# Kernel tuning notes

Measured on AMD Instinct MI355X. Metric: run time of the kernel, lower is better.

## Reference

```python
import jax, jax.numpy as jnp
import numpy as np

H = 8
NUM_GRAPHS = 128
EDGE_DIM = 147

def _glorot(k, shape, fan_in):
    return jax.random.normal(k, shape, jnp.float32) * (1.0 / np.sqrt(fan_in))

def setup_inputs():
    ks = jax.random.split(jax.random.key(0), 28)
    N, E = 50000, 200000
    inp = {}
    inp['x'] = jax.random.normal(ks[0], (N, 64), jnp.float32)
    inp['edge_attr'] = jax.random.uniform(ks[1], (E, EDGE_DIM), dtype=jnp.float32)
    dims = [(64, 64), (512, 64), (512, 32)]  # (in_channels, per-head out) per GATConv layer
    ki = 2
    for i in range(3):
        cin, c = dims[i]
        hc = H * c
        inp['W%d' % i] = _glorot(ks[ki], (hc, cin), cin); ki += 1
        inp['We%d' % i] = _glorot(ks[ki], (hc, EDGE_DIM), EDGE_DIM); ki += 1
        inp['as%d' % i] = _glorot(ks[ki], (1, H, c), c); ki += 1
        inp['ad%d' % i] = _glorot(ks[ki], (1, H, c), c); ki += 1
        inp['ae%d' % i] = _glorot(ks[ki], (1, H, c), c); ki += 1
        inp['b%d' % i] = jnp.zeros((hc,), jnp.float32); ki += 1
    inp['Wc'] = _glorot(ks[ki], (32, 256), 256)
    inp['bc'] = jnp.zeros((32,), jnp.float32)
    inp['edge_index'] = jax.random.randint(ks[ki + 1], (2, E), 0, N)
    inp['batch'] = jnp.sort(jax.random.randint(ks[ki + 2], (N,), 0, NUM_GRAPHS))
    return inp

def _gat_layer(x, src, dst, ea, W, We, a_s, a_d, a_e, b):
    # PyG GATConv (concat=True, eval mode): project, per-edge attention logits,
    # softmax over incoming edges of each destination node, weighted scatter-sum, bias.
    N = x.shape[0]
    HC = W.shape[0]
    C = HC // H
    xp = (x @ W.T).reshape(N, H, C)              # [N,H,C]
    ep = (ea @ We.T).reshape(-1, H, C)           # [E,H,C]
    logits = (xp * a_s).sum(-1)[src] + (xp * a_d).sum(-1)[dst] + (ep * a_e).sum(-1)
    logits = jax.nn.leaky_relu(logits, 0.2)      # [E,H]
    mx = jax.ops.segment_max(logits, dst, num_segments=N)
    mx = jnp.where(jnp.isfinite(mx), mx, 0.0)
    ex = jnp.exp(logits - mx[dst])
    denom = jax.ops.segment_sum(ex, dst, num_segments=N)
    attn = ex / (denom[dst] + 1e-16)             # [E,H]
    out = jax.ops.segment_sum(xp[src] * attn[:, :, None], dst, num_segments=N)
    return out.reshape(N, HC) + b

def _forward(x, edge_attr, params, Wc, bc, edge_index, batch):
    N = x.shape[0]
    src, dst = edge_index[0], edge_index[1]
    # GATConv add_self_loops=True, fill_value='mean': self-loop edge attr is
    # the per-node mean of incoming edge attrs (0 for isolated nodes).
    ones_e = jnp.ones((src.shape[0],), x.dtype)
    deg = jax.ops.segment_sum(ones_e, dst, num_segments=N)
    loop_attr = jax.ops.segment_sum(edge_attr, dst, num_segments=N) / jnp.clip(deg, 1.0)[:, None]
    ar = jnp.arange(N)
    src_f = jnp.concatenate([src, ar])
    dst_f = jnp.concatenate([dst, ar])
    ea_f = jnp.concatenate([edge_attr, loop_attr], axis=0)
    h = x
    for i, p in enumerate(params):
        h = _gat_layer(h, src_f, dst_f, ea_f, *p)
        if i < len(params) - 1:
            h = jax.nn.elu(h)  # dropout is identity in eval
    # batch indices are sorted and contiguous, so the unique->contiguous remap
    # in the original forward is the identity; global mean pool:
    cnt = jax.ops.segment_sum(jnp.ones((N,), h.dtype), batch, num_segments=NUM_GRAPHS)
    pooled = jax.ops.segment_sum(h, batch, num_segments=NUM_GRAPHS) / jnp.clip(cnt, 1.0)[:, None]
    return pooled @ Wc.T + bc

def reference(x, edge_attr, W0, We0, as0, ad0, ae0, b0, W1, We1, as1, ad1, ae1, b1, W2, We2, as2, ad2, ae2, b2, Wc, bc, edge_index, batch):
    params = [(W0, We0, as0, ad0, ae0, b0), (W1, We1, as1, ad1, ae1, b1), (W2, We2, as2, ad2, ae2, b2)]
    return _forward(x, edge_attr, params, Wc, bc, edge_index, batch)
```

## Files before the change

### kernel.cpp

```cpp
#include <hip/hip_runtime.h>
#include <hip/hip_bf16.h>
#include <math.h>

typedef __attribute__((ext_vector_type(8))) _Float16 f16x8;
typedef __attribute__((ext_vector_type(4))) _Float16 f16x4;
typedef __attribute__((ext_vector_type(4))) float f32x4;

#define AS1(p) ((const __attribute__((address_space(1))) void*)(p))
#define AS3(p) ((__attribute__((address_space(3))) void*)(p))

__device__ __forceinline__ float leaky02(float x){ return x > 0.f ? x : 0.2f*x; }
__device__ __forceinline__ ushort f2h(float f){ _Float16 h = (_Float16)f; return *(ushort*)&h; }
__device__ __forceinline__ float h2f(ushort u){ _Float16 h = *(_Float16*)&u; return (float)h; }

__global__ void count_kernel(const int* __restrict__ dst, int* __restrict__ cnt, int E){
  int e = blockIdx.x*blockDim.x + threadIdx.x;
  if (e < E) atomicAdd(&cnt[dst[e]], 1);
}

__global__ void scanA_kernel(const int* __restrict__ cnt, int* __restrict__ bsum, int N){
  __shared__ int sd[256];
  int i = blockIdx.x*256 + threadIdx.x;
  sd[threadIdx.x] = (i<N) ? cnt[i] : 0;
  __syncthreads();
  for (int off=128; off>0; off>>=1){
    if (threadIdx.x < off) sd[threadIdx.x] += sd[threadIdx.x+off];
    __syncthreads();
  }
  if (threadIdx.x==0) bsum[blockIdx.x] = sd[0];
}
__global__ void scanB_kernel(int* __restrict__ bsum, int B){
  __shared__ int sd[256];
  int t = threadIdx.x;
  int v = (t<B) ? bsum[t] : 0;
  sd[t] = v;
  __syncthreads();
  for (int off=1; off<256; off<<=1){
    int u = (t>=off) ? sd[t-off] : 0;
    __syncthreads();
    sd[t] += u;
    __syncthreads();
  }
  if (t<B) bsum[t] = sd[t] - v;
}
__global__ void scanC_kernel(const int* __restrict__ cnt, const int* __restrict__ bsum,
                             int* __restrict__ row_ptr, int N){
  __shared__ int sd[256];
  int i = blockIdx.x*256 + threadIdx.x;
  int v = (i<N) ? cnt[i] : 0;
  sd[threadIdx.x] = v;
  __syncthreads();
  for (int off=1; off<256; off<<=1){
    int u = (threadIdx.x>=off) ? sd[threadIdx.x-off] : 0;
    __syncthreads();
    sd[threadIdx.x] += u;
    __syncthreads();
  }
  if (i < N) row_ptr[i+1] = sd[threadIdx.x] + bsum[blockIdx.x];
  if (i == 0) row_ptr[0] = 0;
}

__global__ void scatter_kernel(const int* __restrict__ src, const int* __restrict__ dst,
                               const int* __restrict__ row_ptr, int* __restrict__ cursor,
                               int* __restrict__ epos, int* __restrict__ csr_src, int E){
  int e = blockIdx.x*blockDim.x + threadIdx.x;
  if (e < E){
    int d = dst[e];
    int pos = row_ptr[d] + atomicAdd(&cursor[d], 1);
    epos[e] = pos;
    csr_src[pos] = src[e];
  }
}

__global__ void conv4_kernel(const float* __restrict__ p0, const float* __restrict__ p1,
                             const float* __restrict__ p2, const float* __restrict__ p3,
                             ushort* __restrict__ q0, ushort* __restrict__ q1,
                             ushort* __restrict__ q2, ushort* __restrict__ q3,
                             int n0, int n1, int n2, int n3){
  int i = blockIdx.x*256 + threadIdx.x;
  const float* src; ushort* dst; int loc;
  if (i < n0){ src=p0; dst=q0; loc=i; }
  else if (i < n0+n1){ src=p1; dst=q1; loc=i-n0; }
  else if (i < n0+n1+n2){ src=p2; dst=q2; loc=i-n0-n1; }
  else if (i < n0+n1+n2+n3){ src=p3; dst=q3; loc=i-n0-n1-n2; }
  else return;
  float4 v = reinterpret_cast<const float4*>(src)[loc];
  ushort4 o; o.x=f2h(v.x); o.y=f2h(v.y); o.z=f2h(v.z); o.w=f2h(v.w);
  reinterpret_cast<ushort4*>(dst)[loc] = o;
}

__global__ void wfold_direct_kernel(const float* __restrict__ We0, const float* __restrict__ ae0,
                                    const float* __restrict__ We1, const float* __restrict__ ae1,
                                    const float* __restrict__ We2, const float* __restrict__ ae2,
                                    ushort* __restrict__ Bh){
  int t = blockIdx.x*256 + threadIdx.x;
  if (t >= 32*160) return;
  int j = t/160, d = t%160;
  float s = 0.f;
  if (j < 24 && d < 147){
    int l = j >> 3, h = j & 7;
    const float* We = (l==0) ? We0 : (l==1) ? We1 : We2;
    const float* ae = (l==0) ? ae0 : (l==1) ? ae1 : ae2;
    int C = (l==2) ? 32 : 64;
    for (int c=0;c<C;c++) s = fmaf(We[(size_t)(h*C+c)*147 + d], ae[h*C+c], s);
  }
  Bh[t] = f2h(s);
}

__global__ __launch_bounds__(256) void edge_alpha_mfma_kernel(const float* __restrict__ ea, const ushort* __restrict__ Bh,
                                                              const int* __restrict__ epos,
                                                              float* __restrict__ aEc, int E){
  int wave = threadIdx.x>>6, lane = threadIdx.x&63;
  int fr = lane&15, fq = lane>>4;
  int m0 = blockIdx.x*64 + wave*16;
  f32x4 acc0 = {0.f,0.f,0.f,0.f}, acc1 = {0.f,0.f,0.f,0.f};
  int row = m0 + fr; if (row > E-1) row = E-1;
  const float*  ar = ea + (size_t)row*147;
  const ushort* b0 = Bh + (size_t)fr*160      + fq*8;
  const ushort* b1 = Bh + (size_t)(16+fr)*160 + fq*8;
  #pragma unroll
  for (int k=0;k<160;k+=32){
    int c0 = k + fq*8;
    f16x8 a;
    #pragma unroll
    for (int u=0;u<8;u++){
      float v = (c0+u < 147) ? ar[c0+u] : 0.f;
      a[u] = (_Float16)v;
    }
    f16x8 p = *(const f16x8*)(b0 + k);
    f16x8 q = *(const f16x8*)(b1 + k);
    acc0 = __builtin_amdgcn_mfma_f32_16x16x32_f16(a, p, acc0, 0, 0, 0);
    acc1 = __builtin_amdgcn_mfma_f32_16x16x32_f16(a, q, acc1, 0, 0, 0);
  }
  #pragma unroll
  for (int j=0;j<4;j++){
    int r = m0 + fq*4 + j;
    if (r < E){
      int p = epos[r];
      aEc[(size_t)p*24 + fr] = acc0[j];
      if (fr < 8) aEc[(size_t)p*24 + 16 + fr] = acc1[j];
    }
  }
}

__global__ __launch_bounds__(192) void loop_alpha_all_kernel(const float* __restrict__ aEc, const int* __restrict__ row_ptr,
                                                             float* __restrict__ loopAE, int N){
  int n = blockIdx.x*8 + threadIdx.x/24;
  int j = threadIdx.x%24;
  if (n >= N) return;
  int row = row_ptr[n], end = row_ptr[n+1];
  float s = 0.f;
  for (int i=row;i<end;i++) s += aEc[(size_t)i*24 + j];
  loopAE[(size_t)n*24 + j] = s / fmaxf((float)(end-row), 1.0f);
}

template<int CPH>
__global__ __launch_bounds__(256) void gemm_mfma_kernel(const ushort* __restrict__ A, const ushort* __restrict__ B,
                                                        ushort* __restrict__ C,
                                                        const float* __restrict__ a_s, const float* __restrict__ a_d,
                                                        float* __restrict__ alphaS, float* __restrict__ alphaD,
                                                        int M, int Nn, int K, int NY){
  __shared__ ushort lds[128*64*4];
  int nwg = gridDim.x;
  int bid = blockIdx.x;
  int q8 = nwg >> 3, r8 = nwg & 7;
  int xcd = bid & 7, loc = bid >> 3;
  int swz = (xcd < r8 ? xcd*(q8+1) : r8*(q8+1) + (xcd-r8)*q8) + loc;
  int m0 = (swz / NY) * 128, n0 = (swz % NY) * 128;

  int wave = threadIdx.x >> 6, lane = threadIdx.x & 63;
  int wr = wave >> 1, wc = wave & 1;
  f32x4 acc[4][4];
  #pragma unroll
  for (int m=0;m<4;m++)
    #pragma unroll
    for (int n=0;n<4;n++) acc[m][n] = (f32x4){0.f,0.f,0.f,0.f};

  int lrow = lane >> 3;
  int lcol = lane & 7;
  int srcChunk = lcol ^ lrow;
  int fr = lane & 15;
  int fq = lane >> 4;

  auto stage = [&](int buf, int k0){
    ushort* As = lds + buf*(128*64*2);
    ushort* Bs = As + 128*64;
    #pragma unroll
    for (int qq=0;qq<4;qq++){
      int r = qq*32 + wave*8 + lrow;
      int gr = m0 + r; if (gr > M-1) gr = M-1;
      __builtin_amdgcn_global_load_lds(AS1(A + (size_t)gr*K + k0 + srcChunk*8), AS3(&As[(qq*32 + wave*8)*64]), 16, 0, 0);
      __builtin_amdgcn_global_load_lds(AS1(B + (size_t)(n0 + r)*K + k0 + srcChunk*8), AS3(&Bs[(qq*32 + wave*8)*64]), 16, 0, 0);
    }
  };

  int nt = K >> 6;
  stage(0, 0);
  int buf = 0;
  for (int t=0; t<nt; ++t){
    if (t+1 < nt){
      stage(buf^1, (t+1)<<6);
      asm volatile("s_waitcnt vmcnt(8)" ::: "memory");
    } else {
      asm volatile("s_waitcnt vmcnt(0)" ::: "memory");
    }
    __builtin_amdgcn_s_barrier();
    __builtin_amdgcn_sched_barrier(0);
    const ushort* As = lds + buf*(128*64*2);
    const ushort* Bs = As + 128*64;
    #pragma unroll
    for (int kk=0; kk<64; kk+=32){
      f16x8 a[4], b[4];
      #pragma unroll
      for (int m=0;m<4;m++){
        int Ra = wr*64 + m*16 + fr;
        int ch = ((kk>>3) + fq) ^ (Ra & 7);
        a[m] = *(const f16x8*)&As[Ra*64 + ch*8];
      }
      #pragma unroll
      for (int n=0;n<4;n++){
        int Rb = wc*64 + n*16 + fr;
        int ch = ((kk>>3) + fq) ^ (Rb & 7);
        b[n] = *(const f16x8*)&Bs[Rb*64 + ch*8];
      }
      #pragma unroll
      for (int m=0;m<4;m++)
        #pragma unroll
        for (int n=0;n<4;n++)
          acc[m][n] = __builtin_amdgcn_mfma_f32_16x16x32_f16(a[m], b[n], acc[m][n], 0, 0, 0);
    }
    __builtin_amdgcn_s_barrier();
    buf ^= 1;
  }

  {
    ushort* Cs = lds;
    #pragma unroll
    for (int m=0;m<4;m++)
      #pragma unroll
      for (int j=0;j<4;j++){
        int rr = wr*64 + m*16 + fq*4 + j;
        #pragma unroll
        for (int n=0;n<4;n++)
          Cs[rr*128 + wc*64 + n*16 + fr] = f2h(acc[m][n][j]);
      }
    __builtin_amdgcn_s_barrier();
    int rbase = threadIdx.x >> 4;
    int cc = (threadIdx.x & 15)*8;
    #pragma unroll
    for (int p=0;p<8;p++){
      int rr = p*16 + rbase;
      int grow = m0 + rr;
      if (grow < M)
        *(f16x8*)(C + (size_t)grow*Nn + n0 + cc) = *(const f16x8*)&Cs[rr*128 + cc];
    }
  }

  int colbase = n0 + wc*64;
  if (CPH == 64){
    int head = colbase >> 6;
    float asv[4], adv[4];
    #pragma unroll
    for (int n=0;n<4;n++){ int cih = n*16 + fr; asv[n] = a_s[head*64 + cih]; adv[n] = a_d[head*64 + cih]; }
    #pragma unroll
    for (int m=0;m<4;m++){
      float ps[4] = {0,0,0,0}, pd[4] = {0,0,0,0};
      #pragma unroll
      for (int n=0;n<4;n++)
        #pragma unroll
        for (int j=0;j<4;j++){ ps[j] = fmaf(acc[m][n][j], asv[n], ps[j]); pd[j] = fmaf(acc[m][n][j], adv[n], pd[j]); }
      #pragma unroll
      for (int off=1; off<16; off<<=1)
        #pragma unroll
        for (int j=0;j<4;j++){ ps[j] += __shfl_xor(ps[j], off); pd[j] += __shfl_xor(pd[j], off); }
      if (fr == 0){
        #pragma unroll
        for (int j=0;j<4;j++){
          int row = m0 + wr*64 + m*16 + fq*4 + j;
          if (row < M){ alphaS[(size_t)row*8 + head] = ps[j]; alphaD[(size_t)row*8 + head] = pd[j]; }
        }
      }
    }
  } else {
    int head0 = colbase >> 5;
    float asv[4], adv[4];
    #pragma unroll
    for (int n=0;n<4;n++){
      int h = head0 + (n>>1);
      int cih = (n&1)*16 + fr;
      asv[n] = a_s[h*32 + cih]; adv[n] = a_d[h*32 + cih];
    }
    #pragma unroll
    for (int m=0;m<4;m++){
      float psA[4]={0,0,0,0}, pdA[4]={0,0,0,0}, psB[4]={0,0,0,0}, pdB[4]={0,0,0,0};
      #pragma unroll
      for (int j=0;j<4;j++){
        #pragma unroll
        for (int n=0;n<2;n++){ psA[j] = fmaf(acc[m][n][j], asv[n], psA[j]); pdA[j] = fmaf(acc[m][n][j], adv[n], pdA[j]); }
        #pragma unroll
        for (int n=2;n<4;n++){ psB[j] = fmaf(acc[m][n][j], asv[n], psB[j]); pdB[j] = fmaf(acc[m][n][j], adv[n], pdB[j]); }
      }
      #pragma unroll
      for (int off=1; off<16; off<<=1)
        #pragma unroll
        for (int j=0;j<4;j++){
          psA[j] += __shfl_xor(psA[j], off); pdA[j] += __shfl_xor(pdA[j], off);
          psB[j] += __shfl_xor(psB[j], off); pdB[j] += __shfl_xor(pdB[j], off);
        }
      if (fr == 0){
        #pragma unroll
        for (int j=0;j<4;j++){
          int row = m0 + wr*64 + m*16 + fq*4 + j;
          if (row < M){
            alphaS[(size_t)row*8 + head0]     = psA[j]; alphaD[(size_t)row*8 + head0]     = pdA[j];
            alphaS[(size_t)row*8 + head0 + 1] = psB[j]; alphaD[(size_t)row*8 + head0 + 1] = pdB[j];
          }
        }
      }
    }
  }
}

template<int V> struct vecT;
template<> struct vecT<8>{ typedef f16x8 T; };
template<> struct vecT<4>{ typedef f16x4 T; };

template<int V>
__device__ __forceinline__ void rowfma(typename vecT<V>::T v, float ex, float* acc){
  #pragma unroll
  for (int j=0;j<V;j++) acc[j] = fmaf(ex, (float)v[j], acc[j]);
}

template<int HC, int ELU>
__global__ __launch_bounds__(256) void aggregate_kernel(
    const ushort* __restrict__ xh, const float* __restrict__ alphaS, const float* __restrict__ alphaD,
    const float* __restrict__ aEc, const float* __restrict__ loopAE,
    const int* __restrict__ row_ptr, const int* __restrict__ csr_src,
    const float* __restrict__ bias, ushort* __restrict__ out, int N, int off){
  constexpr int V = HC/64;
  typedef typename vecT<V>::T vec;
  int w = blockIdx.x*4 + (threadIdx.x>>6);
  int nA = w*2, nB = w*2+1;
  if (nA >= N) return;
  bool hasB = (nB < N);
  int lane = threadIdx.x & 63;
  int h = lane >> 3;
  int cofs = V*lane;

  float adnA = alphaD[(size_t)nA*8 + h];
  float accA[V], accB[V];
  float denA, denB = 0.f;
  {
    float exs = __expf(leaky02(alphaS[(size_t)nA*8 + h] + adnA + loopAE[(size_t)nA*24 + off + h]));
    denA = exs;
    #pragma unroll
    for (int j=0;j<V;j++) accA[j] = 0.f;
    rowfma<V>(*(const vec*)(xh + (size_t)nA*HC + cofs), exs, accA);
  }
  #pragma unroll
  for (int j=0;j<V;j++) accB[j] = 0.f;
  float adnB = 0.f;
  int iA = row_ptr[nA], eAe = row_ptr[nA+1];
  int iB = eAe, eBe = eAe;
  if (hasB){
    adnB = alphaD[(size_t)nB*8 + h];
    float exs = __expf(leaky02(alphaS[(size_t)nB*8 + h] + adnB + loopAE[(size_t)nB*24 + off + h]));
    denB = exs;
    rowfma<V>(*(const vec*)(xh + (size_t)nB*HC + cofs), exs, accB);
    eBe = row_ptr[nB+1];
  }

  bool run = (iA+1 < eAe) && (iB+1 < eBe);
  int sA0=0,sA1=0,sB0=0,sB1=0;
  float gA0=0,gA1=0,gB0=0,gB1=0, tA0=0,tA1=0,tB0=0,tB1=0;
  vec vA0{}, vA1{}, vB0{}, vB1{};
  if (run){
    sA0=csr_src[iA]; sA1=csr_src[iA+1]; sB0=csr_src[iB]; sB1=csr_src[iB+1];
    gA0=alphaS[(size_t)sA0*8+h]; gA1=alphaS[(size_t)sA1*8+h];
    gB0=alphaS[(size_t)sB0*8+h]; gB1=alphaS[(size_t)sB1*8+h];
    tA0=aEc[(size_t)iA*24+off+h]; tA1=aEc[(size_t)(iA+1)*24+off+h];
    tB0=aEc[(size_t)iB*24+off+h]; tB1=aEc[(size_t)(iB+1)*24+off+h];
    vA0=*(const vec*)(xh+(size_t)sA0*HC+cofs); vA1=*(const vec*)(xh+(size_t)sA1*HC+cofs);
    vB0=*(const vec*)(xh+(size_t)sB0*HC+cofs); vB1=*(const vec*)(xh+(size_t)sB1*HC+cofs);
  }
  while (run){
    int jA = iA+2, jB = iB+2;
    bool nrun = (jA+1 < eAe) && (jB+1 < eBe);
    vec cA0=vA0, cA1=vA1, cB0=vB0, cB1=vB1;
    float eA0=__expf(leaky02(gA0+adnA+tA0));
    float eA1=__expf(leaky02(gA1+adnA+tA1));
    float eB0=__expf(leaky02(gB0+adnB+tB0));
    float eB1=__expf(leaky02(gB1+adnB+tB1));
    if (nrun){
      sA0=csr_src[jA]; sA1=csr_src[jA+1]; sB0=csr_src[jB]; sB1=csr_src[jB+1];
      gA0=alphaS[(size_t)sA0*8+h]; gA1=alphaS[(size_t)sA1*8+h];
      gB0=alphaS[(size_t)sB0*8+h]; gB1=alphaS[(size_t)sB1*8+h];
      tA0=aEc[(size_t)jA*24+off+h]; tA1=aEc[(size_t)(jA+1)*24+off+h];
      tB0=aEc[(size_t)jB*24+off+h]; tB1=aEc[(size_t)(jB+1)*24+off+h];
      vA0=*(const vec*)(xh+(size_t)sA0*HC+cofs); vA1=*(const vec*)(xh+(size_t)sA1*HC+cofs);
      vB0=*(const vec*)(xh+(size_t)sB0*HC+cofs); vB1=*(const vec*)(xh+(size_t)sB1*HC+cofs);
    }
    denA += eA0 + eA1; denB += eB0 + eB1;
    rowfma<V>(cA0, eA0, accA); rowfma<V>(cA1, eA1, accA);
    rowfma<V>(cB0, eB0, accB); rowfma<V>(cB1, eB1, accB);
    iA = jA; iB = jB;
    run = nrun;
  }
  for (; iA+1 < eAe; iA += 2){
    int s0 = csr_src[iA], s1 = csr_src[iA+1];
    float g0 = alphaS[(size_t)s0*8+h], g1 = alphaS[(size_t)s1*8+h];
    float t0 = aEc[(size_t)iA*24+off+h], t1 = aEc[(size_t)(iA+1)*24+off+h];
    vec v0 = *(const vec*)(xh+(size_t)s0*HC+cofs);
    vec v1 = *(const vec*)(xh+(size_t)s1*HC+cofs);
    float e0 = __expf(leaky02(g0+adnA+t0));
    float e1 = __expf(leaky02(g1+adnA+t1));
    denA += e0 + e1;
    rowfma<V>(v0, e0, accA); rowfma<V>(v1, e1, accA);
  }
  if (iA < eAe){
    int s = csr_src[iA];
    float g = alphaS[(size_t)s*8+h];
    float t = aEc[(size_t)iA*24+off+h];
    vec v = *(const vec*)(xh+(size_t)s*HC+cofs);
    float e = __expf(leaky02(g+adnA+t));
    denA += e;
    rowfma<V>(v, e, accA);
  }
  for (; iB+1 < eBe; iB += 2){
    int s0 = csr_src[iB], s1 = csr_src[iB+1];
    float g0 = alphaS[(size_t)s0*8+h], g1 = alphaS[(size_t)s1*8+h];
    float t0 = aEc[(size_t)iB*24+off+h], t1 = aEc[(size_t)(iB+1)*24+off+h];
    vec v0 = *(const vec*)(xh+(size_t)s0*HC+cofs);
    vec v1 = *(const vec*)(xh+(size_t)s1*HC+cofs);
    float e0 = __expf(leaky02(g0+adnB+t0));
    float e1 = __expf(leaky02(g1+adnB+t1));
    denB += e0 + e1;
    rowfma<V>(v0, e0, accB); rowfma<V>(v1, e1, accB);
  }
  if (iB < eBe){
    int s = csr_src[iB];
    float g = alphaS[(size_t)s*8+h];
    float t = aEc[(size_t)iB*24+off+h];
    vec v = *(const vec*)(xh+(size_t)s*HC+cofs);
    float e = __expf(leaky02(g+adnB+t));
    denB += e;
    rowfma<V>(v, e, accB);
  }

  float invA = 1.f/(denA + 1e-16f);
  {
    vec ov;
    #pragma unroll
    for (int j=0;j<V;j++){
      float o = accA[j]*invA + bias[cofs + j];
      if (ELU) o = (o > 0.f) ? o : (__expf(o) - 1.f);
      ov[j] = (_Float16)o;
    }
    *(vec*)(out + (size_t)nA*HC + cofs) = ov;
  }
  if (hasB){
    float invB = 1.f/(denB + 1e-16f);
    vec ov;
    #pragma unroll
    for (int j=0;j<V;j++){
      float o = accB[j]*invB + bias[cofs + j];
      if (ELU) o = (o > 0.f) ? o : (__expf(o) - 1.f);
      ov[j] = (_Float16)o;
    }
    *(vec*)(out + (size_t)nB*HC + cofs) = ov;
  }
}

__global__ __launch_bounds__(256) void pool_sum_kernel(const ushort* __restrict__ h, const int* __restrict__ batch,
                                                       float* __restrict__ pooled, int N){
  __shared__ int bsh[128];
  int i0 = blockIdx.x*128;
  int i1 = min(i0+128, N);
  if (threadIdx.x < i1-i0) bsh[threadIdx.x] = batch[i0+threadIdx.x];
  __syncthreads();
  int c = threadIdx.x;
  int gprev = bsh[0];
  float s = 0.f;
  for (int i=i0;i<i1;i++){
    int g = bsh[i-i0];
    if (g != gprev){ atomicAdd(&pooled[gprev*256 + c], s); s = 0.f; gprev = g; }
    s += h2f(h[(size_t)i*256 + c]);
  }
  atomicAdd(&pooled[gprev*256 + c], s);
}

__device__ __forceinline__ int lower_bound_i(const int* a, int n, int key){
  int lo=0, hi=n;
  while (lo<hi){ int mid=(lo+hi)>>1; if (a[mid]<key) lo=mid+1; else hi=mid; }
  return lo;
}

__global__ void final_kernel(const float* __restrict__ pooled, const int* __restrict__ batch,
                             const float* __restrict__ Wc, const float* __restrict__ bc,
                             float* __restrict__ out, int N){
  int g = blockIdx.x; int j = threadIdx.x;
  if (j >= 32) return;
  int start = lower_bound_i(batch, N, g);
  int end   = lower_bound_i(batch, N, g+1);
  float invc = 1.f / fmaxf((float)(end-start), 1.f);
  const float* p = pooled + g*256;
  const float* w = Wc + (size_t)j*256;
  float s = 0.f;
  for (int c=0;c<256;c++) s = fmaf(p[c], w[c], s);
  out[g*32 + j] = s*invc + bc[j];
}

extern "C" void kernel_launch(void* const* d_in, const int* in_sizes, int n_in,
                              void* d_out, int out_size, void* d_ws, size_t ws_size,
                              hipStream_t stream){
  (void)n_in; (void)out_size; (void)ws_size;
  const float* x   = (const float*)d_in[0];
  const float* ea  = (const float*)d_in[1];
  const float* Wt[3]  = {(const float*)d_in[2],  (const float*)d_in[8],  (const float*)d_in[14]};
  const float* Wet[3] = {(const float*)d_in[3],  (const float*)d_in[9],  (const float*)d_in[15]};
  const float* ast[3] = {(const float*)d_in[4],  (const float*)d_in[10], (const float*)d_in[16]};
  const float* adt[3] = {(const float*)d_in[5],  (const float*)d_in[11], (const float*)d_in[17]};
  const float* aet[3] = {(const float*)d_in[6],  (const float*)d_in[12], (const float*)d_in[18]};
  const float* bt[3]  = {(const float*)d_in[7],  (const float*)d_in[13], (const float*)d_in[19]};
  const float* Wc  = (const float*)d_in[20];
  const float* bc  = (const float*)d_in[21];
  const int* ei    = (const int*)d_in[22];
  const int* batch = (const int*)d_in[23];
  int N = in_sizes[0] / 64;
  int E = in_sizes[1] / 147;
  const int* srcp = ei;
  const int* dstp = ei + E;

  char* w = (char*)d_ws;
  size_t off = 0;
  auto carve = [&](size_t bytes)->char*{ char* p = w + off; off += (bytes + 255) & ~(size_t)255; return p; };
  ushort* xh     = (ushort*)carve((size_t)N*512*2);
  ushort* hb     = (ushort*)carve((size_t)N*512*2);
  ushort* xb     = (ushort*)carve((size_t)N*64*2);
  ushort* Wb[3];
  Wb[0] = (ushort*)carve((size_t)512*64*2);
  Wb[1] = (ushort*)carve((size_t)512*512*2);
  Wb[2] = (ushort*)carve((size_t)256*512*2);
  ushort* wfBh   = (ushort*)carve((size_t)32*160*2);
  float*  aEc    = (float*) carve((size_t)E*24*4);
  float*  loopAE = (float*) carve((size_t)N*24*4);
  float*  alphaS = (float*) carve((size_t)N*8*4);
  float*  alphaD = (float*) carve((size_t)N*8*4);
  int*    row_ptr= (int*)   carve((size_t)(N+1)*4);
  int*    epos   = (int*)   carve((size_t)E*4);
  int*    csr_src= (int*)   carve((size_t)E*4);
  int*    bsum   = (int*)   carve((size_t)256*4);
  char*   zbase  = carve(0);
  float*  pooled = (float*) carve((size_t)128*256*4);
  int*    cnt    = (int*)   carve((size_t)N*4);
  int*    cursor = (int*)   carve((size_t)N*4);
  char*   zend   = carve(0);

  hipMemsetAsync(zbase, 0, (size_t)(zend - zbase), stream);

  int nscan = (N+255)/256;
  count_kernel  <<<(E+255)/256, 256, 0, stream>>>(dstp, cnt, E);
  scanA_kernel  <<<nscan, 256, 0, stream>>>(cnt, bsum, N);
  scanB_kernel  <<<1, 256, 0, stream>>>(bsum, nscan);
  scanC_kernel  <<<nscan, 256, 0, stream>>>(cnt, bsum, row_ptr, N);
  scatter_kernel<<<(E+255)/256, 256, 0, stream>>>(srcp, dstp, row_ptr, cursor, epos, csr_src, E);

  wfold_direct_kernel<<<(32*160+255)/256, 256, 0, stream>>>(Wet[0], aet[0], Wet[1], aet[1], Wet[2], aet[2], wfBh);

  conv4_kernel<<<(N*16 + 8192 + 65536 + 32768 + 255)/256, 256, 0, stream>>>(
      x, Wt[0], Wt[1], Wt[2], xb, Wb[0], Wb[1], Wb[2], N*16, 8192, 65536, 32768);

  edge_alpha_mfma_kernel<<<(E+63)/64, 256, 0, stream>>>(ea, wfBh, epos, aEc, E);
  loop_alpha_all_kernel <<<(N+7)/8, 192, 0, stream>>>(aEc, row_ptr, loopAE, N);

  const int HCs[3]  = {512, 512, 256};
  const int CINs[3] = {64, 512, 512};
  int nrow = (N+127)/128;
  for (int l=0; l<3; l++){
    int HC = HCs[l], CIN = CINs[l];
    const ushort* Ain = (l==0) ? xb : hb;
    int NY = HC/128;
    int nwg = nrow * NY;
    if (HC==512) gemm_mfma_kernel<64><<<nwg, 256, 0, stream>>>(Ain, Wb[l], xh, ast[l], adt[l], alphaS, alphaD, N, HC, CIN, NY);
    else         gemm_mfma_kernel<32><<<nwg, 256, 0, stream>>>(Ain, Wb[l], xh, ast[l], adt[l], alphaS, alphaD, N, HC, CIN, NY);
    int ablocks = (N + 7) / 8;
    if (l==0)
      aggregate_kernel<512,1><<<ablocks, 256, 0, stream>>>(xh, alphaS, alphaD, aEc, loopAE, row_ptr, csr_src, bt[l], hb, N, 0);
    else if (l==1)
      aggregate_kernel<512,1><<<ablocks, 256, 0, stream>>>(xh, alphaS, alphaD, aEc, loopAE, row_ptr, csr_src, bt[l], hb, N, 8);
    else
      aggregate_kernel<256,0><<<ablocks, 256, 0, stream>>>(xh, alphaS, alphaD, aEc, loopAE, row_ptr, csr_src, bt[l], hb, N, 16);
  }
  pool_sum_kernel<<<(N+127)/128, 256, 0, stream>>>(hb, batch, pooled, N);
  final_kernel<<<128, 64, 0, stream>>>(pooled, batch, Wc, bc, (float*)d_out, N);
}
```

Baseline: 423.7 us.

## Aggregate layer-0 in 64-dim input space before projecting with per-head GEMM

For the first GAT layer, the attention source/destination logits are computed from folded vectors (W0^T a_s, W0^T a_d) applied to the 64-dim input. Per-edge exponentials are precomputed, and messages are aggregated over the raw 64-dim features per head instead of the 512-dim projected features. A block-diagonal MFMA GEMM then applies each head's projection with bias and ELU. This cuts gather traffic in layer 0 by reading 64-wide rows instead of 512-wide ones. The cost is extra kernels, a csr_dst array, and the skipped max subtraction in the softmax, which risks overflow for large logits.

```diff
diff --git a/kernel.cpp b/kernel.cpp
--- a/kernel.cpp
+++ b/kernel.cpp
@@ -62,13 +62,15 @@
 
 __global__ void scatter_kernel(const int* __restrict__ src, const int* __restrict__ dst,
                                const int* __restrict__ row_ptr, int* __restrict__ cursor,
-                               int* __restrict__ epos, int* __restrict__ csr_src, int E){
+                               int* __restrict__ epos, int* __restrict__ csr_src,
+                               int* __restrict__ csr_dst, int E){
   int e = blockIdx.x*blockDim.x + threadIdx.x;
   if (e < E){
     int d = dst[e];
     int pos = row_ptr[d] + atomicAdd(&cursor[d], 1);
     epos[e] = pos;
     csr_src[pos] = src[e];
+    csr_dst[pos] = d;
   }
 }
 
@@ -107,6 +109,37 @@
   Bh[t] = f2h(s);
 }
 
+__global__ void fold_vsd_kernel(const float* __restrict__ W0, const float* __restrict__ a_s,
+                                const float* __restrict__ a_d, float* __restrict__ vs, float* __restrict__ vd){
+  int t = blockIdx.x*256 + threadIdx.x;
+  if (t >= 512) return;
+  int h = t>>6, d = t&63;
+  float ss=0.f, sd=0.f;
+  for (int c=0;c<64;c++){
+    float w = W0[(size_t)(h*64+c)*64 + d];
+    ss = fmaf(w, a_s[h*64+c], ss);
+    sd = fmaf(w, a_d[h*64+c], sd);
+  }
+  vs[t]=ss; vd[t]=sd;
+}
+
+__global__ void alpha_sd_x_kernel(const ushort* __restrict__ xb, const float* __restrict__ vs, const float* __restrict__ vd,
+                                  float* __restrict__ alphaS, float* __restrict__ alphaD, int N){
+  int t = blockIdx.x*256 + threadIdx.x;
+  if (t >= N*8) return;
+  int n = t>>3, h = t&7;
+  const ushort* xr = xb + (size_t)n*64;
+  const float* vsr = vs + h*64;
+  const float* vdr = vd + h*64;
+  float ss=0.f, sd=0.f;
+  for (int d0=0; d0<64; d0+=8){
+    f16x8 v = *(const f16x8*)(xr + d0);
+    #pragma unroll
+    for (int u=0;u<8;u++){ float f = (float)v[u]; ss = fmaf(f, vsr[d0+u], ss); sd = fmaf(f, vdr[d0+u], sd); }
+  }
+  alphaS[t]=ss; alphaD[t]=sd;
+}
+
 __global__ __launch_bounds__(256) void edge_alpha_mfma_kernel(const float* __restrict__ ea, const ushort* __restrict__ Bh,
                                                               const int* __restrict__ epos,
                                                               float* __restrict__ aEc, int E){
@@ -152,6 +185,147 @@
   float s = 0.f;
   for (int i=row;i<end;i++) s += aEc[(size_t)i*24 + j];
   loopAE[(size_t)n*24 + j] = s / fmaxf((float)(end-row), 1.0f);
+}
+
+__global__ __launch_bounds__(256) void edge_exp_kernel(
+    const float* __restrict__ alphaS, const float* __restrict__ alphaD,
+    const float* __restrict__ aEc, const float* __restrict__ loopAE,
+    const int* __restrict__ csr_src, const int* __restrict__ csr_dst,
+    float* __restrict__ exv_csr, float* __restrict__ selfEx,
+    int E, int N, int off){
+  int t = blockIdx.x*256 + threadIdx.x;
+  if (t < E*8){
+    int i = t >> 3, h = t & 7;
+    int s = csr_src[i], n = csr_dst[i];
+    float v = leaky02(alphaS[(size_t)s*8+h] + alphaD[(size_t)n*8+h] + aEc[(size_t)i*24 + off + h]);
+    exv_csr[t] = __expf(v);
+  } else if (t < (E+N)*8){
+    int u = t - E*8;
+    int n = u >> 3, h = u & 7;
+    float v = leaky02(alphaS[(size_t)n*8+h] + alphaD[(size_t)n*8+h] + loopAE[(size_t)n*24 + off + h]);
+    selfEx[u] = __expf(v);
+  }
+}
+
+__device__ __forceinline__ void acc8(const float4& lo, const float4& hi, float xv, float* acc, float* den){
+  acc[0]=fmaf(lo.x,xv,acc[0]); acc[1]=fmaf(lo.y,xv,acc[1]); acc[2]=fmaf(lo.z,xv,acc[2]); acc[3]=fmaf(lo.w,xv,acc[3]);
+  acc[4]=fmaf(hi.x,xv,acc[4]); acc[5]=fmaf(hi.y,xv,acc[5]); acc[6]=fmaf(hi.z,xv,acc[6]); acc[7]=fmaf(hi.w,xv,acc[7]);
+  den[0]+=lo.x; den[1]+=lo.y; den[2]+=lo.z; den[3]+=lo.w;
+  den[4]+=hi.x; den[5]+=hi.y; den[6]+=hi.z; den[7]+=hi.w;
+}
+
+__global__ __launch_bounds__(256) void aggregate_in_kernel(
+    const ushort* __restrict__ xb, const float* __restrict__ exv, const float* __restrict__ selfEx,
+    const int* __restrict__ row_ptr, const int* __restrict__ csr_src,
+    ushort* __restrict__ agg, int N){
+  int w = blockIdx.x*4 + (threadIdx.x>>6);
+  int nA = w*2, nB = w*2+1;
+  if (nA >= N) return;
+  bool hasB = (nB < N);
+  int d = threadIdx.x & 63;
+  float accA[8], accB[8], denA[8], denB[8];
+  {
+    float4 e0 = *(const float4*)&selfEx[(size_t)nA*8];
+    float4 e1 = *(const float4*)&selfEx[(size_t)nA*8+4];
+    float xs = h2f(xb[(size_t)nA*64 + d]);
+    #pragma unroll
+    for (int h=0;h<8;h++){ accA[h]=0.f; denA[h]=0.f; }
+    acc8(e0, e1, xs, accA, denA);
+  }
+  #pragma unroll
+  for (int h=0;h<8;h++){ accB[h]=0.f; denB[h]=0.f; }
+  if (hasB){
+    float4 e0 = *(const float4*)&selfEx[(size_t)nB*8];
+    float4 e1 = *(const float4*)&selfEx[(size_t)nB*8+4];
+    float xs = h2f(xb[(size_t)nB*64 + d]);
+    acc8(e0, e1, xs, accB, denB);
+  }
+  int iA = row_ptr[nA], eA = row_ptr[nA+1];
+  int iB = eA, eB = eA;
+  if (hasB) eB = row_ptr[nB+1];
+  while (iA+1 < eA && iB+1 < eB){
+    int sA0=csr_src[iA], sA1=csr_src[iA+1], sB0=csr_src[iB], sB1=csr_src[iB+1];
+    float xA0=h2f(xb[(size_t)sA0*64+d]), xA1=h2f(xb[(size_t)sA1*64+d]);
+    float xB0=h2f(xb[(size_t)sB0*64+d]), xB1=h2f(xb[(size_t)sB1*64+d]);
+    float4 a00=*(const float4*)&exv[(size_t)iA*8],     a01=*(const float4*)&exv[(size_t)iA*8+4];
+    float4 a10=*(const float4*)&exv[(size_t)(iA+1)*8], a11=*(const float4*)&exv[(size_t)(iA+1)*8+4];
+    float4 b00=*(const float4*)&exv[(size_t)iB*8],     b01=*(const float4*)&exv[(size_t)iB*8+4];
+    float4 b10=*(const float4*)&exv[(size_t)(iB+1)*8], b11=*(const float4*)&exv[(size_t)(iB+1)*8+4];
+    acc8(a00, a01, xA0, accA, denA); acc8(a10, a11, xA1, accA, denA);
+    acc8(b00, b01, xB0, accB, denB); acc8(b10, b11, xB1, accB, denB);
+    iA += 2; iB += 2;
+  }
+  for (; iA+1 < eA; iA += 2){
+    int s0=csr_src[iA], s1=csr_src[iA+1];
+    float x0=h2f(xb[(size_t)s0*64+d]), x1=h2f(xb[(size_t)s1*64+d]);
+    float4 a0=*(const float4*)&exv[(size_t)iA*8],     a1=*(const float4*)&exv[(size_t)iA*8+4];
+    float4 c0=*(const float4*)&exv[(size_t)(iA+1)*8], c1=*(const float4*)&exv[(size_t)(iA+1)*8+4];
+    acc8(a0, a1, x0, accA, denA); acc8(c0, c1, x1, accA, denA);
+  }
+  if (iA < eA){
+    int s=csr_src[iA];
+    float x0=h2f(xb[(size_t)s*64+d]);
+    float4 a0=*(const float4*)&exv[(size_t)iA*8], a1=*(const float4*)&exv[(size_t)iA*8+4];
+    acc8(a0, a1, x0, accA, denA);
+  }
+  for (; iB+1 < eB; iB += 2){
+    int s0=csr_src[iB], s1=csr_src[iB+1];
+    float x0=h2f(xb[(size_t)s0*64+d]), x1=h2f(xb[(size_t)s1*64+d]);
+    float4 a0=*(const float4*)&exv[(size_t)iB*8],     a1=*(const float4*)&exv[(size_t)iB*8+4];
+    float4 c0=*(const float4*)&exv[(size_t)(iB+1)*8], c1=*(const float4*)&exv[(size_t)(iB+1)*8+4];
+    acc8(a0, a1, x0, accB, denB); acc8(c0, c1, x1, accB, denB);
+  }
+  if (iB < eB){
+    int s=csr_src[iB];
+    float x0=h2f(xb[(size_t)s*64+d]);
+    float4 a0=*(const float4*)&exv[(size_t)iB*8], a1=*(const float4*)&exv[(size_t)iB*8+4];
+    acc8(a0, a1, x0, accB, denB);
+  }
+  #pragma unroll
+  for (int h=0;h<8;h++)
+    agg[(size_t)nA*512 + h*64 + d] = f2h(accA[h] / (denA[h] + 1e-16f));
+  if (hasB){
+    #pragma unroll
+    for (int h=0;h<8;h++)
+      agg[(size_t)nB*512 + h*64 + d] = f2h(accB[h] / (denB[h] + 1e-16f));
+  }
+}
+
+__global__ __launch_bounds__(256) void bd_gemm_kernel(const ushort* __restrict__ agg, const ushort* __restrict__ W0,
+                                                      const float* __restrict__ b0, ushort* __restrict__ out, int N){
+  int head = blockIdx.y;
+  int wave = threadIdx.x>>6, lane = threadIdx.x&63;
+  int fr = lane&15, fq = lane>>4;
+  int r0 = blockIdx.x*64 + wave*16;
+  f32x4 acc[4];
+  #pragma unroll
+  for (int ct=0;ct<4;ct++) acc[ct] = (f32x4){0.f,0.f,0.f,0.f};
+  int arow = r0 + fr; if (arow > N-1) arow = N-1;
+  const ushort* abase = agg + (size_t)arow*512 + head*64 + fq*8;
+  const ushort* bbase = W0 + (size_t)(head*64)*64 + fq*8;
+  #pragma unroll
+  for (int kk=0; kk<64; kk+=32){
+    f16x8 a = *(const f16x8*)(abase + kk);
+    #pragma unroll
+    for (int ct=0; ct<4; ct++){
+      f16x8 b = *(const f16x8*)(bbase + (size_t)(ct*16+fr)*64 + kk);
+      acc[ct] = __builtin_amdgcn_mfma_f32_16x16x32_f16(a, b, acc[ct], 0, 0, 0);
+    }
+  }
+  #pragma unroll
+  for (int ct=0;ct<4;ct++){
+    int col = head*64 + ct*16 + fr;
+    float bb = b0[col];
+    #pragma unroll
+    for (int j=0;j<4;j++){
+      int row = r0 + fq*4 + j;
+      if (row < N){
+        float o = acc[ct][j] + bb;
+        o = (o > 0.f) ? o : (__expf(o) - 1.f);
+        out[(size_t)row*512 + col] = f2h(o);
+      }
+    }
+  }
 }
 
 template<int CPH>
@@ -546,9 +720,14 @@
   float*  loopAE = (float*) carve((size_t)N*24*4);
   float*  alphaS = (float*) carve((size_t)N*8*4);
   float*  alphaD = (float*) carve((size_t)N*8*4);
+  float*  exv    = (float*) carve((size_t)E*8*4);
+  float*  selfEx = (float*) carve((size_t)N*8*4);
+  float*  vs     = (float*) carve((size_t)8*64*4);
+  float*  vd     = (float*) carve((size_t)8*64*4);
   int*    row_ptr= (int*)   carve((size_t)(N+1)*4);
   int*    epos   = (int*)   carve((size_t)E*4);
   int*    csr_src= (int*)   carve((size_t)E*4);
+  int*    csr_dst= (int*)   carve((size_t)E*4);
   int*    bsum   = (int*)   carve((size_t)256*4);
   char*   zbase  = carve(0);
   float*  pooled = (float*) carve((size_t)128*256*4);
@@ -563,9 +742,10 @@
   scanA_kernel  <<<nscan, 256, 0, stream>>>(cnt, bsum, N);
   scanB_kernel  <<<1, 256, 0, stream>>>(bsum, nscan);
   scanC_kernel  <<<nscan, 256, 0, stream>>>(cnt, bsum, row_ptr, N);
-  scatter_kernel<<<(E+255)/256, 256, 0, stream>>>(srcp, dstp, row_ptr, cursor, epos, csr_src, E);
+  scatter_kernel<<<(E+255)/256, 256, 0, stream>>>(srcp, dstp, row_ptr, cursor, epos, csr_src, csr_dst, E);
 
   wfold_direct_kernel<<<(32*160+255)/256, 256, 0, stream>>>(Wet[0], aet[0], Wet[1], aet[1], Wet[2], aet[2], wfBh);
+  fold_vsd_kernel<<<2, 256, 0, stream>>>(Wt[0], ast[0], adt[0], vs, vd);
 
   conv4_kernel<<<(N*16 + 8192 + 65536 + 32768 + 255)/256, 256, 0, stream>>>(
       x, Wt[0], Wt[1], Wt[2], xb, Wb[0], Wb[1], Wb[2], N*16, 8192, 65536, 32768);
@@ -573,20 +753,22 @@
   edge_alpha_mfma_kernel<<<(E+63)/64, 256, 0, stream>>>(ea, wfBh, epos, aEc, E);
   loop_alpha_all_kernel <<<(N+7)/8, 192, 0, stream>>>(aEc, row_ptr, loopAE, N);
 
-  const int HCs[3]  = {512, 512, 256};
-  const int CINs[3] = {64, 512, 512};
+  alpha_sd_x_kernel<<<(N*8+255)/256, 256, 0, stream>>>(xb, vs, vd, alphaS, alphaD, N);
+  int nexp = ((E+N)*8 + 255)/256;
+  edge_exp_kernel<<<nexp, 256, 0, stream>>>(alphaS, alphaD, aEc, loopAE, csr_src, csr_dst, exv, selfEx, E, N, 0);
+  aggregate_in_kernel<<<(N+7)/8, 256, 0, stream>>>(xb, exv, selfEx, row_ptr, csr_src, xh, N);
+  dim3 bdg((N+63)/64, 8);
+  bd_gemm_kernel<<<bdg, 256, 0, stream>>>(xh, Wb[0], bt[0], hb, N);
+
   int nrow = (N+127)/128;
-  for (int l=0; l<3; l++){
-    int HC = HCs[l], CIN = CINs[l];
-    const ushort* Ain = (l==0) ? xb : hb;
+  for (int l=1; l<3; l++){
+    int HC = (l==1) ? 512 : 256, CIN = 512;
     int NY = HC/128;
     int nwg = nrow * NY;
-    if (HC==512) gemm_mfma_kernel<64><<<nwg, 256, 0, stream>>>(Ain, Wb[l], xh, ast[l], adt[l], alphaS, alphaD, N, HC, CIN, NY);
-    else         gemm_mfma_kernel<32><<<nwg, 256, 0, stream>>>(Ain, Wb[l], xh, ast[l], adt[l], alphaS, alphaD, N, HC, CIN, NY);
+    if (HC==512) gemm_mfma_kernel<64><<<nwg, 256, 0, stream>>>(hb, Wb[l], xh, ast[l], adt[l], alphaS, alphaD, N, HC, CIN, NY);
+    else         gemm_mfma_kernel<32><<<nwg, 256, 0, stream>>>(hb, Wb[l], xh, ast[l], adt[l], alphaS, alphaD, N, HC, CIN, NY);
     int ablocks = (N + 7) / 8;
-    if (l==0)
-      aggregate_kernel<512,1><<<ablocks, 256, 0, stream>>>(xh, alphaS, alphaD, aEc, loopAE, row_ptr, csr_src, bt[l], hb, N, 0);
-    else if (l==1)
+    if (l==1)
       aggregate_kernel<512,1><<<ablocks, 256, 0, stream>>>(xh, alphaS, alphaD, aEc, loopAE, row_ptr, csr_src, bt[l], hb, N, 8);
     else
       aggregate_kernel<256,0><<<ablocks, 256, 0, stream>>>(xh, alphaS, alphaD, aEc, loopAE, row_ptr, csr_src, bt[l], hb, N, 16);
```

New measurement: 474.8 us. +12.1%, slower.

## Enlarge GEMM block tile to 256x128 rows with eight waves per block

Applied to the files above, without the earlier changes.

The projection GEMM now processes 256 output rows per workgroup with 512 threads (8 waves), so each staged B tile is reused across twice as many A rows. The global-to-LDS staging is rewritten for the new thread count, the LDS buffer grows to hold the larger A tile, and the wait count is adjusted to match. The C write-back now goes out in two halves through a padded LDS stride. In exchange, the grid has half as many workgroups, occupancy per CU may drop because of the larger LDS footprint, and the epilogue needs extra barriers.

```diff
diff --git a/kernel.cpp b/kernel.cpp
--- a/kernel.cpp
+++ b/kernel.cpp
@@ -155,18 +155,18 @@
 }
 
 template<int CPH>
-__global__ __launch_bounds__(256) void gemm_mfma_kernel(const ushort* __restrict__ A, const ushort* __restrict__ B,
+__global__ __launch_bounds__(512) void gemm_mfma_kernel(const ushort* __restrict__ A, const ushort* __restrict__ B,
                                                         ushort* __restrict__ C,
                                                         const float* __restrict__ a_s, const float* __restrict__ a_d,
                                                         float* __restrict__ alphaS, float* __restrict__ alphaD,
                                                         int M, int Nn, int K, int NY){
-  __shared__ ushort lds[128*64*4];
+  __shared__ ushort lds[2*24576];
   int nwg = gridDim.x;
   int bid = blockIdx.x;
   int q8 = nwg >> 3, r8 = nwg & 7;
   int xcd = bid & 7, loc = bid >> 3;
   int swz = (xcd < r8 ? xcd*(q8+1) : r8*(q8+1) + (xcd-r8)*q8) + loc;
-  int m0 = (swz / NY) * 128, n0 = (swz % NY) * 128;
+  int m0 = (swz / NY) * 256, n0 = (swz % NY) * 128;
 
   int wave = threadIdx.x >> 6, lane = threadIdx.x & 63;
   int wr = wave >> 1, wc = wave & 1;
@@ -176,21 +176,24 @@
     #pragma unroll
     for (int n=0;n<4;n++) acc[m][n] = (f32x4){0.f,0.f,0.f,0.f};
 
-  int lrow = lane >> 3;
-  int lcol = lane & 7;
-  int srcChunk = lcol ^ lrow;
   int fr = lane & 15;
   int fq = lane >> 4;
 
   auto stage = [&](int buf, int k0){
-    ushort* As = lds + buf*(128*64*2);
-    ushort* Bs = As + 128*64;
-    #pragma unroll
-    for (int qq=0;qq<4;qq++){
-      int r = qq*32 + wave*8 + lrow;
-      int gr = m0 + r; if (gr > M-1) gr = M-1;
-      __builtin_amdgcn_global_load_lds(AS1(A + (size_t)gr*K + k0 + srcChunk*8), AS3(&As[(qq*32 + wave*8)*64]), 16, 0, 0);
-      __builtin_amdgcn_global_load_lds(AS1(B + (size_t)(n0 + r)*K + k0 + srcChunk*8), AS3(&Bs[(qq*32 + wave*8)*64]), 16, 0, 0);
+    ushort* As = lds + buf*24576;
+    ushort* Bs = As + 16384;
+    #pragma unroll
+    for (int q=0;q<4;q++){
+      int idx = q*512 + threadIdx.x;
+      int row = idx>>3, ch = (idx&7) ^ (row&7);
+      int gr = m0 + row; if (gr > M-1) gr = M-1;
+      __builtin_amdgcn_global_load_lds(AS1(A + (size_t)gr*K + k0 + ch*8), AS3(&As[(size_t)idx*8]), 16, 0, 0);
+    }
+    #pragma unroll
+    for (int q=0;q<2;q++){
+      int idx = q*512 + threadIdx.x;
+      int row = idx>>3, ch = (idx&7) ^ (row&7);
+      __builtin_amdgcn_global_load_lds(AS1(B + (size_t)(n0+row)*K + k0 + ch*8), AS3(&Bs[(size_t)idx*8]), 16, 0, 0);
     }
   };
 
@@ -200,14 +203,14 @@
   for (int t=0; t<nt; ++t){
     if (t+1 < nt){
       stage(buf^1, (t+1)<<6);
-      asm volatile("s_waitcnt vmcnt(8)" ::: "memory");
+      asm volatile("s_waitcnt vmcnt(6)" ::: "memory");
     } else {
       asm volatile("s_waitcnt vmcnt(0)" ::: "memory");
     }
     __builtin_amdgcn_s_barrier();
     __builtin_amdgcn_sched_barrier(0);
-    const ushort* As = lds + buf*(128*64*2);
-    const ushort* Bs = As + 128*64;
+    const ushort* As = lds + buf*24576;
+    const ushort* Bs = As + 16384;
     #pragma unroll
     for (int kk=0; kk<64; kk+=32){
       f16x8 a[4], b[4];
@@ -236,23 +239,30 @@
   {
     ushort* Cs = lds;
     #pragma unroll
-    for (int m=0;m<4;m++)
-      #pragma unroll
-      for (int j=0;j<4;j++){
-        int rr = wr*64 + m*16 + fq*4 + j;
-        #pragma unroll
-        for (int n=0;n<4;n++)
-          Cs[rr*128 + wc*64 + n*16 + fr] = f2h(acc[m][n][j]);
+    for (int half=0; half<2; half++){
+      __syncthreads();
+      if ((wr>>1) == half){
+        int lr0 = (wr&1)*64;
+        #pragma unroll
+        for (int m=0;m<4;m++)
+          #pragma unroll
+          for (int j=0;j<4;j++){
+            int rr = lr0 + m*16 + fq*4 + j;
+            #pragma unroll
+            for (int n=0;n<4;n++)
+              Cs[rr*136 + wc*64 + n*16 + fr] = f2h(acc[m][n][j]);
+          }
       }
-    __builtin_amdgcn_s_barrier();
-    int rbase = threadIdx.x >> 4;
-    int cc = (threadIdx.x & 15)*8;
-    #pragma unroll
-    for (int p=0;p<8;p++){
-      int rr = p*16 + rbase;
-      int grow = m0 + rr;
-      if (grow < M)
-        *(f16x8*)(C + (size_t)grow*Nn + n0 + cc) = *(const f16x8*)&Cs[rr*128 + cc];
+      __syncthreads();
+      int r = threadIdx.x >> 4;
+      int cc = (threadIdx.x & 15)*8;
+      #pragma unroll
+      for (int p=0;p<4;p++){
+        int rr = p*32 + r;
+        int grow = m0 + half*128 + rr;
+        if (grow < M)
+          *(f16x8*)(C + (size_t)grow*Nn + n0 + cc) = *(const f16x8*)&Cs[rr*136 + cc];
+      }
     }
   }
 
@@ -575,14 +585,14 @@
 
   const int HCs[3]  = {512, 512, 256};
   const int CINs[3] = {64, 512, 512};
-  int nrow = (N+127)/128;
+  int nrow = (N+255)/256;
   for (int l=0; l<3; l++){
     int HC = HCs[l], CIN = CINs[l];
     const ushort* Ain = (l==0) ? xb : hb;
     int NY = HC/128;
     int nwg = nrow * NY;
-    if (HC==512) gemm_mfma_kernel<64><<<nwg, 256, 0, stream>>>(Ain, Wb[l], xh, ast[l], adt[l], alphaS, alphaD, N, HC, CIN, NY);
-    else         gemm_mfma_kernel<32><<<nwg, 256, 0, stream>>>(Ain, Wb[l], xh, ast[l], adt[l], alphaS, alphaD, N, HC, CIN, NY);
+    if (HC==512) gemm_mfma_kernel<64><<<nwg, 512, 0, stream>>>(Ain, Wb[l], xh, ast[l], adt[l], alphaS, alphaD, N, HC, CIN, NY);
+    else         gemm_mfma_kernel<32><<<nwg, 512, 0, stream>>>(Ain, Wb[l], xh, ast[l], adt[l], alphaS, alphaD, N, HC, CIN, NY);
     int ablocks = (N + 7) / 8;
     if (l==0)
       aggregate_kernel<512,1><<<ablocks, 256, 0, stream>>>(xh, alphaS, alphaD, aEc, loopAE, row_ptr, csr_src, bt[l], hb, N, 0);
```

After: 435.8 us. +2.8%, slower.

## Load GEMM B fragments directly from global memory and pad C staging tile

Applied to the files above, without the earlier changes.

The MFMA GEMM no longer stages the B (weight) tile in LDS. Each wave now reads its B fragments straight from global memory, relying on cache since the weights are small and reused across blocks. This halves LDS traffic and footprint, which may raise occupancy, and the A staging is reindexed per thread. The output staging tile uses a padded row stride to cut bank conflicts. The cost is per-iteration global load latency for B, which is not prefetched or double-buffered and could stall the MFMAs.

```diff
diff --git a/kernel.cpp b/kernel.cpp
--- a/kernel.cpp
+++ b/kernel.cpp
@@ -160,7 +160,7 @@
                                                         const float* __restrict__ a_s, const float* __restrict__ a_d,
                                                         float* __restrict__ alphaS, float* __restrict__ alphaD,
                                                         int M, int Nn, int K, int NY){
-  __shared__ ushort lds[128*64*4];
+  __shared__ ushort lds[17408];
   int nwg = gridDim.x;
   int bid = blockIdx.x;
   int q8 = nwg >> 3, r8 = nwg & 7;
@@ -176,41 +176,41 @@
     #pragma unroll
     for (int n=0;n<4;n++) acc[m][n] = (f32x4){0.f,0.f,0.f,0.f};
 
-  int lrow = lane >> 3;
-  int lcol = lane & 7;
-  int srcChunk = lcol ^ lrow;
   int fr = lane & 15;
   int fq = lane >> 4;
 
   auto stage = [&](int buf, int k0){
-    ushort* As = lds + buf*(128*64*2);
-    ushort* Bs = As + 128*64;
-    #pragma unroll
-    for (int qq=0;qq<4;qq++){
-      int r = qq*32 + wave*8 + lrow;
-      int gr = m0 + r; if (gr > M-1) gr = M-1;
-      __builtin_amdgcn_global_load_lds(AS1(A + (size_t)gr*K + k0 + srcChunk*8), AS3(&As[(qq*32 + wave*8)*64]), 16, 0, 0);
-      __builtin_amdgcn_global_load_lds(AS1(B + (size_t)(n0 + r)*K + k0 + srcChunk*8), AS3(&Bs[(qq*32 + wave*8)*64]), 16, 0, 0);
+    ushort* As = lds + buf*8192;
+    #pragma unroll
+    for (int q=0;q<4;q++){
+      int idx = q*256 + threadIdx.x;
+      int row = idx>>3, ch = (idx&7) ^ (row&7);
+      int gr = m0 + row; if (gr > M-1) gr = M-1;
+      __builtin_amdgcn_global_load_lds(AS1(A + (size_t)gr*K + k0 + ch*8), AS3(&As[(size_t)idx*8]), 16, 0, 0);
     }
   };
 
+  const ushort* Bq = B + (size_t)(n0 + wc*64)*K;
   int nt = K >> 6;
   stage(0, 0);
   int buf = 0;
   for (int t=0; t<nt; ++t){
     if (t+1 < nt){
       stage(buf^1, (t+1)<<6);
-      asm volatile("s_waitcnt vmcnt(8)" ::: "memory");
+      asm volatile("s_waitcnt vmcnt(4)" ::: "memory");
     } else {
       asm volatile("s_waitcnt vmcnt(0)" ::: "memory");
     }
     __builtin_amdgcn_s_barrier();
     __builtin_amdgcn_sched_barrier(0);
-    const ushort* As = lds + buf*(128*64*2);
-    const ushort* Bs = As + 128*64;
+    const ushort* As = lds + buf*8192;
+    int k0 = t<<6;
     #pragma unroll
     for (int kk=0; kk<64; kk+=32){
       f16x8 a[4], b[4];
+      #pragma unroll
+      for (int n=0;n<4;n++)
+        b[n] = *(const f16x8*)(Bq + (size_t)(n*16 + fr)*K + k0 + kk + fq*8);
       #pragma unroll
       for (int m=0;m<4;m++){
         int Ra = wr*64 + m*16 + fr;
@@ -218,12 +218,6 @@
         a[m] = *(const f16x8*)&As[Ra*64 + ch*8];
       }
       #pragma unroll
-      for (int n=0;n<4;n++){
-        int Rb = wc*64 + n*16 + fr;
-        int ch = ((kk>>3) + fq) ^ (Rb & 7);
-        b[n] = *(const f16x8*)&Bs[Rb*64 + ch*8];
-      }
-      #pragma unroll
       for (int m=0;m<4;m++)
         #pragma unroll
         for (int n=0;n<4;n++)
@@ -242,17 +236,17 @@
         int rr = wr*64 + m*16 + fq*4 + j;
         #pragma unroll
         for (int n=0;n<4;n++)
-          Cs[rr*128 + wc*64 + n*16 + fr] = f2h(acc[m][n][j]);
+          Cs[rr*136 + wc*64 + n*16 + fr] = f2h(acc[m][n][j]);
       }
     __builtin_amdgcn_s_barrier();
-    int rbase = threadIdx.x >> 4;
+    int r = threadIdx.x >> 4;
     int cc = (threadIdx.x & 15)*8;
     #pragma unroll
     for (int p=0;p<8;p++){
-      int rr = p*16 + rbase;
+      int rr = p*16 + r;
       int grow = m0 + rr;
       if (grow < M)
-        *(f16x8*)(C + (size_t)grow*Nn + n0 + cc) = *(const f16x8*)&Cs[rr*128 + cc];
+        *(f16x8*)(C + (size_t)grow*Nn + n0 + cc) = *(const f16x8*)&Cs[rr*136 + cc];
     }
   }
 
```

Result: slower. 448.3 us (+5.8%).
